# Kernel tuning notes

Hardware: AMD Instinct MI355X
Metric: run time of the kernel (lower is better)

The kernel has to match this reference:

```python
import jax, jax.numpy as jnp
import numpy as np

B, L, D_MODEL = 8, 256, 256
D_STATE, D_INNER, DT_RANK, D_CONV = 16, 512, 16, 4


def _ln(x, g, b, eps):
    mu = x.mean(-1, keepdims=True)
    var = ((x - mu) ** 2).mean(-1, keepdims=True)
    return (x - mu) * jax.lax.rsqrt(var + eps) * g + b


def _ssm(x, W_in, conv_w, conv_b, W_x, W_dt, b_dt, A_log, Dp, W_out):
    # x: (B, L, D_MODEL) -- standard Mamba selective-scan block
    xz = x @ W_in                                  # (B,L,2*Di)
    xc, z = jnp.split(xz, 2, axis=-1)
    K = conv_w.shape[-1]
    xp = jnp.pad(xc, ((0, 0), (K - 1, 0), (0, 0)))  # causal depthwise conv
    xc = sum(xp[:, k:k + L, :] * conv_w[:, k] for k in range(K)) + conv_b
    xc = jax.nn.silu(xc)
    x_dbl = xc @ W_x                               # (B,L,R+2S)
    dt, Bm, Cm = jnp.split(x_dbl, [DT_RANK, DT_RANK + D_STATE], axis=-1)
    dt = jax.nn.softplus(dt @ W_dt + b_dt)         # (B,L,Di)
    A = -jnp.exp(A_log)                            # (Di,S)
    dA = jnp.exp(dt[..., None] * A)                # (B,L,Di,S)
    dBx = dt[..., None] * Bm[:, :, None, :] * xc[..., None]

    def step(h, inp):
        dA_t, dBx_t, C_t = inp
        h = dA_t * h + dBx_t                       # (B,Di,S)
        y = jnp.einsum('bds,bs->bd', h, C_t)
        return h, y

    h0 = jnp.zeros((xc.shape[0], D_INNER, D_STATE), xc.dtype)
    xs = (dA.transpose(1, 0, 2, 3), dBx.transpose(1, 0, 2, 3), Cm.transpose(1, 0, 2))
    _, ys = jax.lax.scan(step, h0, xs)             # (L,B,Di)
    y = ys.transpose(1, 0, 2) + xc * Dp
    y = y * jax.nn.silu(z)
    return y @ W_out


def _basic(x, ln_g, ln_b, ssm_params):
    # Basic_Block: ReLU(SSM(LN(x))) + x  (drop_path=0, attn_drop=0)
    return jax.nn.relu(_ssm(_ln(x, ln_g, ln_b, 1e-6), *ssm_params)) + x


def setup_inputs() -> dict:
    key = jax.random.key(0)
    ks = jax.random.split(key, 32)

    def n(k, shape, s=0.02):
        return jax.random.normal(k, shape, dtype=jnp.float32) * s

    inp = {}
    inp['x_spa'] = jax.random.normal(ks[0], (B, L, D_MODEL), dtype=jnp.float32)
    inp['x_spe'] = jax.random.normal(ks[1], (B, L, D_MODEL), dtype=jnp.float32)
    i = 2
    A_init = jnp.log(jnp.tile(jnp.arange(1, D_STATE + 1, dtype=jnp.float32), (D_INNER, 1)))
    for p in ('spa', 'spe'):
        inp[p + '_ln_g'] = jnp.ones((D_MODEL,), jnp.float32)
        inp[p + '_ln_b'] = jnp.zeros((D_MODEL,), jnp.float32)
        inp[p + '_W_in'] = n(ks[i], (D_MODEL, 2 * D_INNER)); i += 1
        inp[p + '_conv_w'] = n(ks[i], (D_INNER, D_CONV), 0.1); i += 1
        inp[p + '_conv_b'] = jnp.zeros((D_INNER,), jnp.float32)
        inp[p + '_W_x'] = n(ks[i], (D_INNER, DT_RANK + 2 * D_STATE)); i += 1
        inp[p + '_W_dt'] = n(ks[i], (DT_RANK, D_INNER), 0.1); i += 1
        inp[p + '_b_dt'] = n(ks[i], (D_INNER,), 0.1); i += 1
        inp[p + '_A_log'] = A_init
        inp[p + '_D'] = jnp.ones((D_INNER,), jnp.float32)
        inp[p + '_W_out'] = n(ks[i], (D_INNER, D_MODEL)); i += 1
    inp['sc_W'] = n(ks[i], (D_MODEL, D_MODEL)); i += 1
    inp['sc_b'] = jnp.zeros((D_MODEL,), jnp.float32)
    inp['sc_ln_g'] = jnp.ones((D_MODEL,), jnp.float32)
    inp['sc_ln_b'] = jnp.zeros((D_MODEL,), jnp.float32)
    inp['fusion_W'] = n(ks[i], (D_MODEL, D_MODEL))
    return inp


def reference(x_spa, x_spe,
              spa_ln_g, spa_ln_b, spa_W_in, spa_conv_w, spa_conv_b, spa_W_x,
              spa_W_dt, spa_b_dt, spa_A_log, spa_D, spa_W_out,
              spe_ln_g, spe_ln_b, spe_W_in, spe_conv_w, spe_conv_b, spe_W_x,
              spe_W_dt, spe_b_dt, spe_A_log, spe_D, spe_W_out,
              sc_W, sc_b, sc_ln_g, sc_ln_b, fusion_W):
    # shared shortcut: Linear + LayerNorm (eps=1e-5)
    ident_spa = _ln(x_spa @ sc_W + sc_b, sc_ln_g, sc_ln_b, 1e-5)
    ident_spe = _ln(x_spe @ sc_W + sc_b, sc_ln_g, sc_ln_b, 1e-5)
    spa_p = (spa_W_in, spa_conv_w, spa_conv_b, spa_W_x, spa_W_dt, spa_b_dt, spa_A_log, spa_D, spa_W_out)
    spe_p = (spe_W_in, spe_conv_w, spe_conv_b, spe_W_x, spe_W_dt, spe_b_dt, spe_A_log, spe_D, spe_W_out)
    a = _basic(x_spa, spa_ln_g, spa_ln_b, spa_p)
    e = _basic(x_spe, spe_ln_g, spe_ln_b, spe_p)
    # fusion gate: mean-pool both branches, Linear(no bias) + sigmoid, broadcast-mul
    fw = jax.nn.sigmoid(((a.mean(1) + e.mean(1)) * 0.5) @ fusion_W)[:, None, :]
    a = a * fw
    e = e * fw
    return (a + ident_spa, e + ident_spe)
```

## Files before the change

### kernel.cpp

```cpp
#include <hip/hip_runtime.h>
#include <hip/hip_bf16.h>
#include <math.h>

#define BD 8
#define LD 256
#define DM 256
#define DS 16
#define DI 512
#define RK 16

#define NROWS (2*BD*LD)
#define HALF_ROWS (BD*LD)

typedef __attribute__((ext_vector_type(8))) short bhalf8;
typedef __attribute__((ext_vector_type(4))) float f32x4;

__device__ __forceinline__ float siluf(float x){ return x / (1.f + __expf(-x)); }
__device__ __forceinline__ float softplusf(float x){
  return fmaxf(x, 0.f) + log1pf(__expf(-fabsf(x)));
}
__device__ __forceinline__ unsigned short f2bf(float f){
  __hip_bfloat16 h = __float2bfloat16(f);
  return *reinterpret_cast<unsigned short*>(&h);
}


__global__ __launch_bounds__(256) void k_prep(
    const float* __restrict__ Wi_spa, const float* __restrict__ Wi_spe,
    const float* __restrict__ Wo_spa, const float* __restrict__ Wo_spe,
    const float* __restrict__ scW,
    const float* __restrict__ Wx_spa, const float* __restrict__ Wx_spe,
    const float* __restrict__ x_spa, const float* __restrict__ x_spe,
    const float* __restrict__ g_spa, const float* __restrict__ b_spa,
    const float* __restrict__ g_spe, const float* __restrict__ b_spe,
    unsigned short* __restrict__ Wt_i_spa, unsigned short* __restrict__ Wt_i_spe,
    unsigned short* __restrict__ Wt_o_spa, unsigned short* __restrict__ Wt_o_spe,
    unsigned short* __restrict__ scWt,
    unsigned short* __restrict__ Wxt_spa, unsigned short* __restrict__ Wxt_spe,
    unsigned short* __restrict__ xnbf, unsigned short* __restrict__ xbf,
    float* __restrict__ pooled)
{
  __shared__ __align__(16) unsigned char smem[59904];
  int b = blockIdx.x;
  int tid = threadIdx.x;
  if (b == 60){
    for (int i=tid; i<BD*DM; i+=256) pooled[i] = 0.f;
    return;
  }
  if (b >= 61){
    float (*xst)[260] = (float (*)[260])smem;
    float (*red)[16]  = (float (*)[16])(smem + 16640);
    float *mu = (float*)(smem + 17664);
    float *rs = (float*)(smem + 17728);
    int r0g = (b - 61) * 16;
    int branch = r0g >= HALF_ROWS;
    const float* xb = branch ? x_spe : x_spa;
    const float* g  = branch ? g_spe : g_spa;
    const float* be = branch ? b_spe : b_spa;
    int rr0 = branch ? r0g - HALF_ROWS : r0g;
    for (int p=0;p<4;p++){
      int i4 = tid + 256*p;
      int r = i4 >> 6, c4 = (i4 & 63)*4;
      *(float4*)&xst[r][c4] = *(const float4*)(xb + (rr0+r)*DM + c4);
    }
    __syncthreads();
    {
      int row = tid >> 4, seg = tid & 15;
      float s = 0.f, s2 = 0.f;
      #pragma unroll
      for (int i=0;i<4;i++){
        float4 v = *(float4*)&xst[row][seg*16 + i*4];
        s  += v.x+v.y+v.z+v.w;
        s2 += v.x*v.x + v.y*v.y + v.z*v.z + v.w*v.w;
      }
      red[row][seg] = s;
      __syncthreads();
      if (seg == 0){
        float t=0.f;
        #pragma unroll
        for (int i=0;i<16;i++) t += red[row][i];
        mu[row] = t * (1.f/DM);
      }
      __syncthreads();
      red[row][seg] = s2;
      __syncthreads();
      if (seg == 0){
        float t=0.f;
        #pragma unroll
        for (int i=0;i<16;i++) t += red[row][i];
        float m = mu[row];
        rs[row] = rsqrtf(t*(1.f/DM) - m*m + 1e-6f);
      }
    }
    __syncthreads();
    for (int p=0;p<4;p++){
      int i4 = tid + 256*p;
      int r = i4 >> 6, c4 = (i4 & 63)*4;
      float4 v  = *(float4*)&xst[r][c4];
      float4 gv = *(const float4*)(g + c4);
      float4 bv = *(const float4*)(be + c4);
      float m = mu[r], rv = rs[r];
      unsigned int rlo = (unsigned int)f2bf(v.x) | ((unsigned int)f2bf(v.y) << 16);
      unsigned int rhi = (unsigned int)f2bf(v.z) | ((unsigned int)f2bf(v.w) << 16);
      *(uint2*)&xbf[(r0g+r)*DM + c4] = make_uint2(rlo, rhi);
      unsigned int nlo = (unsigned int)f2bf((v.x-m)*rv*gv.x + bv.x)
                       | ((unsigned int)f2bf((v.y-m)*rv*gv.y + bv.y) << 16);
      unsigned int nhi = (unsigned int)f2bf((v.z-m)*rv*gv.z + bv.z)
                       | ((unsigned int)f2bf((v.w-m)*rv*gv.w + bv.w) << 16);
      *(uint2*)&xnbf[(r0g+r)*DM + c4] = make_uint2(nlo, nhi);
    }
    return;
  }
  if (b >= 52){
    int bb = b - 52;
    int branch = bb >> 2, chunk = bb & 3;
    int k0 = chunk*128;
    const float* Wx = branch ? Wx_spe : Wx_spa;
    unsigned short* Wxt = branch ? Wxt_spe : Wxt_spa;
    float (*tile2)[49] = (float (*)[49])(smem + 34816);
    for (int i=tid; i<128*48; i+=256){
      int kk = i/48, c = i - kk*48;
      tile2[kk][c] = Wx[(k0+kk)*48 + c];
    }
    __syncthreads();
    for (int i=tid; i<64*128; i+=256){
      int cc = i >> 7, kk = i & 127;
      float v = (cc < 48) ? tile2[kk][cc] : 0.f;
      int kg = k0 + kk;
      int ct = cc >> 4, m16 = cc & 15;
      int ks = kg >> 5, quad = (kg >> 3) & 3, j = kg & 7;
      Wxt[((ct*16 + ks)*64 + quad*16 + m16)*8 + j] = f2bf(v);
    }
    return;
  }
  unsigned short (*tile)[68] = (unsigned short (*)[68])smem;
  const float* W; unsigned short* Wt; int N, K, c0, k0;
  if (b < 32){
    int bb = b & 15;
    W  = (b < 16) ? Wi_spa  : Wi_spe;
    Wt = (b < 16) ? Wt_i_spa: Wt_i_spe;
    N = 1024; K = 256; c0 = (bb >> 2)*256; k0 = (bb & 3)*64;
  } else if (b < 48){
    int bb = b - 32; int h = bb >> 3; bb &= 7;
    W  = h ? Wo_spe  : Wo_spa;
    Wt = h ? Wt_o_spe: Wt_o_spa;
    N = 256; K = 512; c0 = 0; k0 = bb*64;
  } else {
    int bb = b - 48;
    W = scW; Wt = scWt;
    N = 256; K = 256; c0 = 0; k0 = bb*64;
  }
  int c = c0 + tid;
  #pragma unroll 8
  for (int kk=0; kk<64; kk++)
    tile[tid][kk] = f2bf(W[(k0+kk)*N + c]);
  __syncthreads();
  int ksegs = K >> 5;
  for (int p=0; p<16; p++){
    int i = tid + 256*p;
    int cl = i >> 4, kq = (i & 15)*4;
    int cg = c0 + cl;
    int ct = cg >> 4, m16 = cg & 15;
    int kg = k0 + kq;
    int ks = kg >> 5, quad = (kg >> 3) & 3, j = kg & 7;
    uint2 v = *(const uint2*)&tile[cl][kq];
    *(uint2*)&Wt[((ct*ksegs + ks)*64 + quad*16 + m16)*8 + j] = v;
  }
}

__global__ __launch_bounds__(256) void k_gemm1(
    const unsigned short* __restrict__ xnbf, const unsigned short* __restrict__ xbf,
    const unsigned short* __restrict__ Wt_spa, const unsigned short* __restrict__ Wt_spe,
    const unsigned short* __restrict__ scWt, const float* __restrict__ sc_b,
    const float* __restrict__ ln_g, const float* __restrict__ ln_b,
    float* __restrict__ xc_raw, float* __restrict__ szout, float* __restrict__ ident)
{
  __shared__ unsigned short At[16][264];
  __shared__ float Dt[16][260];
  __shared__ float red[16][16];
  __shared__ float mu[16], rs[16];
  int tid = threadIdx.x;
  int bi = blockIdx.x;
  int w = tid >> 6, lane = tid & 63;
  int m16 = lane & 15, quad = lane >> 4;
  if (bi < 1024){
    int rg = bi >> 2, cg = bi & 3;
    int r0 = rg * 16;
    int branch = (r0 >= HALF_ROWS);
    const unsigned short* Wt = branch ? Wt_spe : Wt_spa;
    for (int p=0;p<2;p++){
      int i = tid + 256*p;
      int r = i >> 5, oct = (i & 31)*8;
      *(uint4*)&At[r][oct] = *(const uint4*)&xnbf[(r0+r)*DM + oct];
    }
    __syncthreads();
    bhalf8 af[8];
    #pragma unroll
    for (int ks=0; ks<8; ks++)
      af[ks] = *(const bhalf8*)&At[m16][ks*32 + quad*8];
    f32x4 acc[4];
    #pragma unroll
    for (int ct=0; ct<4; ct++) acc[ct] = (f32x4)(0.f);
    #pragma unroll
    for (int ks=0; ks<8; ks++){
      #pragma unroll
      for (int ct=0; ct<4; ct++){
        int f = (cg*16 + w*4 + ct)*8 + ks;
        bhalf8 bf = *(const bhalf8*)&Wt[f*512 + lane*8];
        acc[ct] = __builtin_amdgcn_mfma_f32_16x16x32_bf16(af[ks], bf, acc[ct], 0,0,0);
      }
    }
    bool isz = (cg >= 2);
    float* outp = isz ? szout : xc_raw;
    int cbase = (cg & 1)*256 + w*64;
    #pragma unroll
    for (int ct=0; ct<4; ct++){
      #pragma unroll
      for (int e=0;e<4;e++){
        int row = r0 + quad*4 + e;
        int col = cbase + ct*16 + m16;
        float v = acc[ct][e];
        if (isz) v = siluf(v);
        outp[row*DI + col] = v;
      }
    }
  } else {
    int r0 = (bi - 1024) * 16;
    for (int p=0;p<2;p++){
      int i = tid + 256*p;
      int r = i >> 5, oct = (i & 31)*8;
      *(uint4*)&At[r][oct] = *(const uint4*)&xbf[(r0+r)*DM + oct];
    }
    __syncthreads();
    bhalf8 af[8];
    #pragma unroll
    for (int ks=0; ks<8; ks++)
      af[ks] = *(const bhalf8*)&At[m16][ks*32 + quad*8];
    f32x4 acc[4];
    #pragma unroll
    for (int ct=0; ct<4; ct++) acc[ct] = (f32x4)(0.f);
    #pragma unroll
    for (int ks=0; ks<8; ks++){
      #pragma unroll
      for (int ct=0; ct<4; ct++){
        int f = (w*4 + ct)*8 + ks;
        bhalf8 bf = *(const bhalf8*)&scWt[f*512 + lane*8];
        acc[ct] = __builtin_amdgcn_mfma_f32_16x16x32_bf16(af[ks], bf, acc[ct], 0,0,0);
      }
    }
    #pragma unroll
    for (int ct=0; ct<4; ct++){
      #pragma unroll
      for (int e=0;e<4;e++){
        int row = quad*4 + e;
        int col = w*64 + ct*16 + m16;
        Dt[row][col] = acc[ct][e] + sc_b[col];
      }
    }
    __syncthreads();
    {
      int row = tid >> 4, seg = tid & 15;
      float s = 0.f, s2 = 0.f;
      #pragma unroll
      for (int i=0;i<4;i++){
        float4 v = *(const float4*)&Dt[row][seg*16 + i*4];
        s  += v.x+v.y+v.z+v.w;
        s2 += v.x*v.x + v.y*v.y + v.z*v.z + v.w*v.w;
      }
      red[row][seg] = s;
      __syncthreads();
      if (seg == 0){
        float t=0.f;
        #pragma unroll
        for (int i=0;i<16;i++) t += red[row][i];
        mu[row] = t * (1.f/DM);
      }
      __syncthreads();
      red[row][seg] = s2;
      __syncthreads();
      if (seg == 0){
        float t=0.f;
        #pragma unroll
        for (int i=0;i<16;i++) t += red[row][i];
        float m = mu[row];
        rs[row] = rsqrtf(t*(1.f/DM) - m*m + 1e-5f);
      }
    }
    __syncthreads();
    float gg = ln_g[tid], bb2 = ln_b[tid];
    #pragma unroll
    for (int r=0;r<16;r++)
      ident[(r0+r)*DM + tid] = (Dt[r][tid]-mu[r])*rs[r]*gg + bb2;
  }
}

__global__ __launch_bounds__(256) void k_convdbl(
    const float* __restrict__ cw_spa, const float* __restrict__ cb_spa,
    const float* __restrict__ cw_spe, const float* __restrict__ cb_spe,
    const float* __restrict__ xc_raw,
    const unsigned short* __restrict__ Wxt_spa, const unsigned short* __restrict__ Wxt_spe,
    const float* __restrict__ Wdt_spa, const float* __restrict__ bdt_spa,
    const float* __restrict__ Wdt_spe, const float* __restrict__ bdt_spe,
    float* __restrict__ xc, float* __restrict__ dt,
    float* __restrict__ Bm, float* __restrict__ Cm)
{
  __shared__ unsigned short At[16][520];
  __shared__ float xdbl[16][18];
  int tid = threadIdx.x;
  int r0 = blockIdx.x * 16;
  int branch = r0 >= HALF_ROWS;
  int l0 = r0 & (LD-1);
  const float* cw = branch ? cw_spe : cw_spa;
  const float* cb = branch ? cb_spe : cb_spa;
  const unsigned short* Wxt = branch ? Wxt_spe : Wxt_spa;
  const float* Wdt = branch ? Wdt_spe : Wdt_spa;
  const float* bdt = branch ? bdt_spe : bdt_spa;
  {
    int c = tid*2;
    float4 w0 = *(const float4*)(cw + 4*c);
    float4 w1 = *(const float4*)(cw + 4*(c+1));
    float2 bias = *(const float2*)(cb + c);
    float2 h0, h1, h2;
    if (l0 > 0){
      h0 = *(const float2*)(xc_raw + (r0-3)*DI + c);
      h1 = *(const float2*)(xc_raw + (r0-2)*DI + c);
      h2 = *(const float2*)(xc_raw + (r0-1)*DI + c);
    } else {
      h0 = make_float2(0.f,0.f); h1 = h0; h2 = h0;
    }
    #pragma unroll
    for (int r=0;r<16;r++){
      float2 cur = *(const float2*)(xc_raw + (r0+r)*DI + c);
      float vx = bias.x;
      vx = fmaf(h0.x, w0.x, vx); vx = fmaf(h1.x, w0.y, vx);
      vx = fmaf(h2.x, w0.z, vx); vx = fmaf(cur.x, w0.w, vx);
      float vy = bias.y;
      vy = fmaf(h0.y, w1.x, vy); vy = fmaf(h1.y, w1.y, vy);
      vy = fmaf(h2.y, w1.z, vy); vy = fmaf(cur.y, w1.w, vy);
      vx = siluf(vx); vy = siluf(vy);
      *(float2*)(xc + (r0+r)*DI + c) = make_float2(vx, vy);
      unsigned int pk = (unsigned int)f2bf(vx) | ((unsigned int)f2bf(vy) << 16);
      *(unsigned int*)&At[r][c] = pk;
      h0 = h1; h1 = h2; h2 = cur;
    }
  }
  __syncthreads();
  int w = tid >> 6, lane = tid & 63;
  int m16 = lane & 15, quad = lane >> 4;
  f32x4 acc = (f32x4)(0.f);
  #pragma unroll
  for (int ks=0; ks<16; ks++){
    bhalf8 a = *(const bhalf8*)&At[m16][ks*32 + quad*8];
    int f = w*16 + ks;
    bhalf8 bf = *(const bhalf8*)&Wxt[f*512 + lane*8];
    acc = __builtin_amdgcn_mfma_f32_16x16x32_bf16(a, bf, acc, 0,0,0);
  }
  #pragma unroll
  for (int e=0;e<4;e++){
    int row = quad*4 + e;
    float v = acc[e];
    if (w == 0)      xdbl[row][m16] = v;
    else if (w == 1) Bm[(r0+row)*DS + m16] = v;
    else if (w == 2) Cm[(r0+row)*DS + m16] = v;
  }
  __syncthreads();
  float wdt0[16], wdt1[16];
  #pragma unroll
  for (int j=0;j<16;j++){ wdt0[j]=Wdt[j*DI+tid]; wdt1[j]=Wdt[j*DI+tid+256]; }
  float b0 = bdt[tid], b1 = bdt[tid+256];
  #pragma unroll
  for (int r=0;r<16;r++){
    float a0=b0, a1=b1;
    #pragma unroll
    for (int j=0;j<16;j++){
      float xv = xdbl[r][j];
      a0 = fmaf(xv, wdt0[j], a0);
      a1 = fmaf(xv, wdt1[j], a1);
    }
    dt[(r0+r)*DI + tid]       = softplusf(a0);
    dt[(r0+r)*DI + tid + 256] = softplusf(a1);
  }
}

__global__ __launch_bounds__(256) void k_scan(
    const float* __restrict__ Alog_spa, const float* __restrict__ Dp_spa,
    const float* __restrict__ Alog_spe, const float* __restrict__ Dp_spe,
    const float* __restrict__ dt, const float* __restrict__ xc,
    const float* __restrict__ sz, const float* __restrict__ Bm,
    const float* __restrict__ Cm, unsigned short* __restrict__ ybf)
{
  __shared__ float ypbuf[2][16][257];
  __shared__ float Dsh[16];
  int tid = threadIdx.x;
  int bi = blockIdx.x;
  int branch = bi >> 8;
  int rem = bi & 255;
  int b = rem >> 5;
  int d0 = (rem & 31) * 16;
  const float* Alog = branch ? Alog_spe : Alog_spa;
  const float* Dp   = branch ? Dp_spe   : Dp_spa;
  int dg = tid >> 4, s = tid & 15;
  int d = d0 + dg;
  float A_ds = -__expf(Alog[d*DS + s]);
  if (tid < 16) Dsh[tid] = Dp[d0 + tid];
  int row0 = branch*HALF_ROWS + b*LD;
  int wcol = s*16 + ((dg + s) & 15);
  float h = 0.f;
  float rdt[2][16], rxc[2][16], rB[2][16], rC[2][16], rsz[2];
  #pragma unroll
  for (int li=0; li<16; li++){
    rdt[0][li] = dt[(row0+li)*DI + d];
    rxc[0][li] = xc[(row0+li)*DI + d];
    rB[0][li]  = Bm[(row0+li)*DS + s];
    rC[0][li]  = Cm[(row0+li)*DS + s];
  }
  rsz[0] = sz[(row0+s)*DI + d0 + dg];
  #pragma unroll
  for (int c=0; c<16; c++){
    int buf = c & 1, nb = buf ^ 1;
    int rbase = row0 + c*16;
    float yp[16];
    #pragma unroll
    for (int li=0; li<16; li++){
      float dA = __expf(rdt[buf][li] * A_ds);
      h = fmaf(dA, h, rdt[buf][li] * rB[buf][li] * rxc[buf][li]);
      yp[li] = h * rC[buf][li];
    }
    if (c < 15){
      int nbase = rbase + 16;
      #pragma unroll
      for (int li=0; li<16; li++){
        rdt[nb][li] = dt[(nbase+li)*DI + d];
        rxc[nb][li] = xc[(nbase+li)*DI + d];
        rB[nb][li]  = Bm[(nbase+li)*DS + s];
        rC[nb][li]  = Cm[(nbase+li)*DS + s];
      }
      rsz[nb] = sz[(nbase+s)*DI + d0 + dg];
    }
    #pragma unroll
    for (int li=0; li<16; li++)
      ypbuf[buf][li][wcol] = yp[li];
    __syncthreads();
    float acc = 0.f;
    #pragma unroll
    for (int ss=0; ss<16; ss++)
      acc += ypbuf[buf][s][ss*16 + ((dg + ss) & 15)];
    float yv = fmaf(rxc[buf][s], Dsh[dg], acc) * rsz[buf];
    ybf[(rbase+s)*DI + d0 + dg] = f2bf(yv);
  }
}

__global__ __launch_bounds__(256) void k_wout(
    const unsigned short* __restrict__ Wt_spa, const unsigned short* __restrict__ Wt_spe,
    const float* __restrict__ x_spa, const float* __restrict__ x_spe,
    const unsigned short* __restrict__ ybf, float* __restrict__ ae,
    float* __restrict__ pooled)
{
  __shared__ unsigned short At[16][520];
  int tid = threadIdx.x;
  int bi = blockIdx.x;
  int r0 = (bi >> 1) * 16;
  int ch = bi & 1;
  int branch = (r0 >= HALF_ROWS);
  const unsigned short* Wt = branch ? Wt_spe : Wt_spa;
  const float* xb = branch ? x_spe : x_spa;
  int rr0 = branch ? r0 - HALF_ROWS : r0;
  for (int p=0;p<4;p++){
    int i = tid + 256*p;
    int r = i >> 6, oct = (i & 63)*8;
    *(uint4*)&At[r][oct] = *(const uint4*)&ybf[(r0+r)*DI + oct];
  }
  __syncthreads();
  int w = tid >> 6, lane = tid & 63;
  int m16 = lane & 15, quad = lane >> 4;
  bhalf8 af[16];
  #pragma unroll
  for (int ks=0; ks<16; ks++)
    af[ks] = *(const bhalf8*)&At[m16][ks*32 + quad*8];
  f32x4 acc[2];
  #pragma unroll
  for (int ct=0; ct<2; ct++) acc[ct] = (f32x4)(0.f);
  #pragma unroll
  for (int ks=0; ks<16; ks++){
    #pragma unroll
    for (int ct=0; ct<2; ct++){
      int f = (ch*8 + w*2 + ct)*16 + ks;
      bhalf8 bf = *(const bhalf8*)&Wt[f*512 + lane*8];
      acc[ct] = __builtin_amdgcn_mfma_f32_16x16x32_bf16(af[ks], bf, acc[ct], 0,0,0);
    }
  }
  float ps0 = 0.f, ps1 = 0.f;
  #pragma unroll
  for (int ct=0; ct<2; ct++){
    #pragma unroll
    for (int e=0;e<4;e++){
      int row = quad*4 + e;
      int col = ch*128 + w*32 + ct*16 + m16;
      float v = fmaxf(acc[ct][e], 0.f) + xb[(rr0+row)*DM + col];
      ae[(r0+row)*DM + col] = v;
      if (ct == 0) ps0 += v; else ps1 += v;
    }
  }
  ps0 += __shfl_xor(ps0, 16, 64); ps0 += __shfl_xor(ps0, 32, 64);
  ps1 += __shfl_xor(ps1, 16, 64); ps1 += __shfl_xor(ps1, 32, 64);
  if (quad == 0){
    int bidx = (r0 >> 8) & 7;
    atomicAdd(&pooled[bidx*DM + ch*128 + w*32 + m16],      ps0);
    atomicAdd(&pooled[bidx*DM + ch*128 + w*32 + 16 + m16], ps1);
  }
}

__global__ __launch_bounds__(256) void k_gatefinal(const float* __restrict__ pooled,
    const float* __restrict__ fW, const float* __restrict__ ae,
    const float* __restrict__ ident, float* __restrict__ out)
{
  __shared__ float p[DM];
  __shared__ float fwsh[DM];
  int bi = blockIdx.x, c = threadIdx.x;
  int r0 = bi * 32;
  int b = (r0 >> 8) & 7;
  p[c] = pooled[b*DM+c] * (0.5f/LD);
  __syncthreads();
  float a = 0.f;
  for (int k=0;k<DM;k+=4){
    a = fmaf(p[k+0], fW[(k+0)*DM+c], a);
    a = fmaf(p[k+1], fW[(k+1)*DM+c], a);
    a = fmaf(p[k+2], fW[(k+2)*DM+c], a);
    a = fmaf(p[k+3], fW[(k+3)*DM+c], a);
  }
  fwsh[c] = 1.f/(1.f+__expf(-a));
  __syncthreads();
  for (int q=0;q<8;q++){
    int i4 = c + 256*q;
    int r = i4 >> 6, c4 = (i4 & 63)*4;
    int base = (r0 + r)*DM + c4;
    float4 av = *(const float4*)(ae + base);
    float4 iv = *(const float4*)(ident + base);
    float4 fv = *(const float4*)&fwsh[c4];
    float4 o;
    o.x = fmaf(av.x, fv.x, iv.x);
    o.y = fmaf(av.y, fv.y, iv.y);
    o.z = fmaf(av.z, fv.z, iv.z);
    o.w = fmaf(av.w, fv.w, iv.w);
    *(float4*)(out + base) = o;
  }
}

extern "C" void kernel_launch(void* const* d_in, const int* in_sizes, int n_in,
                              void* d_out, int out_size, void* d_ws, size_t ws_size,
                              hipStream_t stream) {
  const float* x_spa     = (const float*)d_in[0];
  const float* x_spe     = (const float*)d_in[1];
  const float* spa_ln_g  = (const float*)d_in[2];
  const float* spa_ln_b  = (const float*)d_in[3];
  const float* spa_W_in  = (const float*)d_in[4];
  const float* spa_cw    = (const float*)d_in[5];
  const float* spa_cb    = (const float*)d_in[6];
  const float* spa_W_x   = (const float*)d_in[7];
  const float* spa_W_dt  = (const float*)d_in[8];
  const float* spa_b_dt  = (const float*)d_in[9];
  const float* spa_A_log = (const float*)d_in[10];
  const float* spa_D     = (const float*)d_in[11];
  const float* spa_W_out = (const float*)d_in[12];
  const float* spe_ln_g  = (const float*)d_in[13];
  const float* spe_ln_b  = (const float*)d_in[14];
  const float* spe_W_in  = (const float*)d_in[15];
  const float* spe_cw    = (const float*)d_in[16];
  const float* spe_cb    = (const float*)d_in[17];
  const float* spe_W_x   = (const float*)d_in[18];
  const float* spe_W_dt  = (const float*)d_in[19];
  const float* spe_b_dt  = (const float*)d_in[20];
  const float* spe_A_log = (const float*)d_in[21];
  const float* spe_D     = (const float*)d_in[22];
  const float* spe_W_out = (const float*)d_in[23];
  const float* sc_W      = (const float*)d_in[24];
  const float* sc_b      = (const float*)d_in[25];
  const float* sc_ln_g   = (const float*)d_in[26];
  const float* sc_ln_b   = (const float*)d_in[27];
  const float* fusion_W  = (const float*)d_in[28];

  float* ws = (float*)d_ws;
  float* ident  = ws;
  float* xc_raw = ident  + NROWS*DM;
  float* sz     = xc_raw + NROWS*DI;
  float* xc     = sz     + NROWS*DI;
  float* dt     = xc     + NROWS*DI;
  float* Bm     = dt     + NROWS*DI;
  float* Cm     = Bm     + NROWS*DS;
  float* pooled = Cm     + NROWS*DS;
  float* fw     = pooled + BD*DM;
  unsigned short* Wt_i_spa = (unsigned short*)(fw + BD*DM);
  unsigned short* Wt_i_spe = Wt_i_spa + 1024*256;
  unsigned short* Wt_o_spa = Wt_i_spe + 1024*256;
  unsigned short* Wt_o_spe = Wt_o_spa + 256*512;
  unsigned short* scWt     = Wt_o_spe + 256*512;
  unsigned short* Wxt_spa  = scWt     + 256*256;
  unsigned short* Wxt_spe  = Wxt_spa  + 64*512;
  unsigned short* xnbf     = Wxt_spe  + 64*512;
  unsigned short* xbf      = xnbf     + NROWS*DM;

  float* out = (float*)d_out;

  k_prep<<<317, 256, 0, stream>>>(spa_W_in, spe_W_in, spa_W_out, spe_W_out, sc_W,
                                  spa_W_x, spe_W_x, x_spa, x_spe,
                                  spa_ln_g, spa_ln_b, spe_ln_g, spe_ln_b,
                                  Wt_i_spa, Wt_i_spe, Wt_o_spa, Wt_o_spe, scWt,
                                  Wxt_spa, Wxt_spe, xnbf, xbf, pooled);
  k_gemm1<<<1280, 256, 0, stream>>>(xnbf, xbf, Wt_i_spa, Wt_i_spe, scWt, sc_b,
                                    sc_ln_g, sc_ln_b, xc_raw, sz, ident);
  k_convdbl<<<NROWS/16, 256, 0, stream>>>(spa_cw, spa_cb, spe_cw, spe_cb, xc_raw,
                                          Wxt_spa, Wxt_spe,
                                          spa_W_dt, spa_b_dt, spe_W_dt, spe_b_dt,
                                          xc, dt, Bm, Cm);
  unsigned short* ybf = (unsigned short*)xc_raw;
  k_scan<<<512, 256, 0, stream>>>(spa_A_log, spa_D, spe_A_log, spe_D, dt, xc, sz, Bm, Cm, ybf);
  float* ae = dt;
  k_wout<<<512, 256, 0, stream>>>(Wt_o_spa, Wt_o_spe, x_spa, x_spe, ybf, ae, pooled);
  k_gatefinal<<<128, 256, 0, stream>>>(pooled, fusion_W, ae, ident, out);
}
```

Measured before the change: 198.0 us.

## Fuse fusion-gate and final output into W_out kernel via grid-wide barrier

Merges the final gating kernel into the W_out GEMM kernel. Each block keeps its outputs in registers, then waits at a software grid barrier built on a global atomic counter until all 512 blocks have added to the pooled sums. It then computes the sigmoid gate for its 128 columns and writes the output directly. This removes one kernel launch and the write and re-read of the intermediate activation, but it relies on all 512 blocks being resident at once, which could deadlock otherwise, and each block redundantly recomputes its part of the gate matvec.

```diff
diff --git a/kernel.cpp b/kernel.cpp
--- a/kernel.cpp
+++ b/kernel.cpp
@@ -38,13 +38,14 @@
     unsigned short* __restrict__ scWt,
     unsigned short* __restrict__ Wxt_spa, unsigned short* __restrict__ Wxt_spe,
     unsigned short* __restrict__ xnbf, unsigned short* __restrict__ xbf,
-    float* __restrict__ pooled)
+    float* __restrict__ pooled, unsigned int* __restrict__ ctr)
 {
   __shared__ __align__(16) unsigned char smem[59904];
   int b = blockIdx.x;
   int tid = threadIdx.x;
   if (b == 60){
     for (int i=tid; i<BD*DM; i+=256) pooled[i] = 0.f;
+    if (tid == 0) *ctr = 0u;
     return;
   }
   if (b >= 61){
@@ -453,10 +454,14 @@
 __global__ __launch_bounds__(256) void k_wout(
     const unsigned short* __restrict__ Wt_spa, const unsigned short* __restrict__ Wt_spe,
     const float* __restrict__ x_spa, const float* __restrict__ x_spe,
-    const unsigned short* __restrict__ ybf, float* __restrict__ ae,
-    float* __restrict__ pooled)
+    const unsigned short* __restrict__ ybf,
+    const float* __restrict__ ident, const float* __restrict__ fW,
+    float* __restrict__ out, float* __restrict__ pooled,
+    unsigned int* __restrict__ ctr)
 {
   __shared__ unsigned short At[16][520];
+  __shared__ float psh[DM];
+  __shared__ float fwsh[128];
   int tid = threadIdx.x;
   int bi = blockIdx.x;
   int r0 = (bi >> 1) * 16;
@@ -489,6 +494,7 @@
       acc[ct] = __builtin_amdgcn_mfma_f32_16x16x32_bf16(af[ks], bf, acc[ct], 0,0,0);
     }
   }
+  float vv[8];
   float ps0 = 0.f, ps1 = 0.f;
   #pragma unroll
   for (int ct=0; ct<2; ct++){
@@ -497,52 +503,48 @@
       int row = quad*4 + e;
       int col = ch*128 + w*32 + ct*16 + m16;
       float v = fmaxf(acc[ct][e], 0.f) + xb[(rr0+row)*DM + col];
-      ae[(r0+row)*DM + col] = v;
+      vv[ct*4+e] = v;
       if (ct == 0) ps0 += v; else ps1 += v;
     }
   }
   ps0 += __shfl_xor(ps0, 16, 64); ps0 += __shfl_xor(ps0, 32, 64);
   ps1 += __shfl_xor(ps1, 16, 64); ps1 += __shfl_xor(ps1, 32, 64);
+  int bidx = (r0 >> 8) & 7;
   if (quad == 0){
-    int bidx = (r0 >> 8) & 7;
     atomicAdd(&pooled[bidx*DM + ch*128 + w*32 + m16],      ps0);
     atomicAdd(&pooled[bidx*DM + ch*128 + w*32 + 16 + m16], ps1);
   }
-}
-
-__global__ __launch_bounds__(256) void k_gatefinal(const float* __restrict__ pooled,
-    const float* __restrict__ fW, const float* __restrict__ ae,
-    const float* __restrict__ ident, float* __restrict__ out)
-{
-  __shared__ float p[DM];
-  __shared__ float fwsh[DM];
-  int bi = blockIdx.x, c = threadIdx.x;
-  int r0 = bi * 32;
-  int b = (r0 >> 8) & 7;
-  p[c] = pooled[b*DM+c] * (0.5f/LD);
-  __syncthreads();
-  float a = 0.f;
-  for (int k=0;k<DM;k+=4){
-    a = fmaf(p[k+0], fW[(k+0)*DM+c], a);
-    a = fmaf(p[k+1], fW[(k+1)*DM+c], a);
-    a = fmaf(p[k+2], fW[(k+2)*DM+c], a);
-    a = fmaf(p[k+3], fW[(k+3)*DM+c], a);
-  }
-  fwsh[c] = 1.f/(1.f+__expf(-a));
-  __syncthreads();
-  for (int q=0;q<8;q++){
-    int i4 = c + 256*q;
-    int r = i4 >> 6, c4 = (i4 & 63)*4;
-    int base = (r0 + r)*DM + c4;
-    float4 av = *(const float4*)(ae + base);
-    float4 iv = *(const float4*)(ident + base);
-    float4 fv = *(const float4*)&fwsh[c4];
-    float4 o;
-    o.x = fmaf(av.x, fv.x, iv.x);
-    o.y = fmaf(av.y, fv.y, iv.y);
-    o.z = fmaf(av.z, fv.z, iv.z);
-    o.w = fmaf(av.w, fv.w, iv.w);
-    *(float4*)(out + base) = o;
+  __threadfence();
+  __syncthreads();
+  if (tid == 0){
+    __hip_atomic_fetch_add(ctr, 1u, __ATOMIC_ACQ_REL, __HIP_MEMORY_SCOPE_AGENT);
+    while (__hip_atomic_load(ctr, __ATOMIC_ACQUIRE, __HIP_MEMORY_SCOPE_AGENT) < 512u) ;
+  }
+  __syncthreads();
+  psh[tid] = pooled[bidx*DM + tid] * (0.5f/LD);
+  __syncthreads();
+  if (tid < 128){
+    int col = ch*128 + tid;
+    float a = 0.f;
+    for (int k=0;k<DM;k+=4){
+      a = fmaf(psh[k+0], fW[(k+0)*DM+col], a);
+      a = fmaf(psh[k+1], fW[(k+1)*DM+col], a);
+      a = fmaf(psh[k+2], fW[(k+2)*DM+col], a);
+      a = fmaf(psh[k+3], fW[(k+3)*DM+col], a);
+    }
+    fwsh[tid] = 1.f/(1.f+__expf(-a));
+  }
+  __syncthreads();
+  #pragma unroll
+  for (int ct=0; ct<2; ct++){
+    #pragma unroll
+    for (int e=0;e<4;e++){
+      int row = quad*4 + e;
+      int lc = w*32 + ct*16 + m16;
+      int col = ch*128 + lc;
+      int base = (r0+row)*DM + col;
+      out[base] = fmaf(vv[ct*4+e], fwsh[lc], ident[base]);
+    }
   }
 }
 
@@ -588,8 +590,8 @@
   float* Bm     = dt     + NROWS*DI;
   float* Cm     = Bm     + NROWS*DS;
   float* pooled = Cm     + NROWS*DS;
-  float* fw     = pooled + BD*DM;
-  unsigned short* Wt_i_spa = (unsigned short*)(fw + BD*DM);
+  unsigned int* ctr = (unsigned int*)(pooled + BD*DM);
+  unsigned short* Wt_i_spa = (unsigned short*)(ctr + 64);
   unsigned short* Wt_i_spe = Wt_i_spa + 1024*256;
   unsigned short* Wt_o_spa = Wt_i_spe + 1024*256;
   unsigned short* Wt_o_spe = Wt_o_spa + 256*512;
@@ -605,7 +607,7 @@
                                   spa_W_x, spe_W_x, x_spa, x_spe,
                                   spa_ln_g, spa_ln_b, spe_ln_g, spe_ln_b,
                                   Wt_i_spa, Wt_i_spe, Wt_o_spa, Wt_o_spe, scWt,
-                                  Wxt_spa, Wxt_spe, xnbf, xbf, pooled);
+                                  Wxt_spa, Wxt_spe, xnbf, xbf, pooled, ctr);
   k_gemm1<<<1280, 256, 0, stream>>>(xnbf, xbf, Wt_i_spa, Wt_i_spe, scWt, sc_b,
                                     sc_ln_g, sc_ln_b, xc_raw, sz, ident);
   k_convdbl<<<NROWS/16, 256, 0, stream>>>(spa_cw, spa_cb, spe_cw, spe_cb, xc_raw,
@@ -614,7 +616,6 @@
                                           xc, dt, Bm, Cm);
   unsigned short* ybf = (unsigned short*)xc_raw;
   k_scan<<<512, 256, 0, stream>>>(spa_A_log, spa_D, spe_A_log, spe_D, dt, xc, sz, Bm, Cm, ybf);
-  float* ae = dt;
-  k_wout<<<512, 256, 0, stream>>>(Wt_o_spa, Wt_o_spe, x_spa, x_spe, ybf, ae, pooled);
-  k_gatefinal<<<128, 256, 0, stream>>>(pooled, fusion_W, ae, ident, out);
-}
+  k_wout<<<512, 256, 0, stream>>>(Wt_o_spa, Wt_o_spe, x_spa, x_spe, ybf,
+                                  ident, fusion_W, out, pooled, ctr);
+}
```

Result: slower. 271.5 us (+37.1%).
